# Performance work log

Hardware: AMD Instinct MI355X
Metric: run time of the kernel (lower is better)

The kernel has to match this reference:

```python
import jax, jax.numpy as jnp
import numpy as np

PATCH_SIZE = 16
PATCH_STRIDE = 8
LEVEL = 3

# pywt db4 decomposition filters (dec_lo, dec_hi)
_DB4_DEC_LO = np.array([-0.010597401784997278, 0.032883011666982945,
                        0.030841381835986965, -0.18703481171888114,
                        -0.02798376941698385, 0.6308807679295904,
                        0.7148465705525415, 0.23037781330885523], dtype=np.float32)
_DB4_DEC_HI = np.array([-0.23037781330885523, 0.7148465705525415,
                        -0.6308807679295904, -0.02798376941698385,
                        0.18703481171888114, 0.030841381835986965,
                        -0.032883011666982945, -0.010597401784997278], dtype=np.float32)


def _swt(x, level):
    """Undecimated (a-trous) SWT with periodic boundary, ptwt convention.
    x: (BN, T) with T divisible by 2**level. Returns [cA_L, cD_L, ..., cD_1]."""
    # torch conv1d is cross-correlation -> use flipped filters (true convolution)
    filt = jnp.stack([jnp.asarray(_DB4_DEC_LO[::-1].copy()),
                      jnp.asarray(_DB4_DEC_HI[::-1].copy())], axis=0)[:, None, :]  # (2,1,8)
    filt = filt.astype(x.dtype)
    flen = filt.shape[-1]
    res_lo = x[:, None, :]  # (BN, 1, T)
    details = []
    for lvl in range(level):
        d = 2 ** lvl
        padl, padr = d * (flen // 2 - 1), d * (flen // 2)
        xp = jnp.concatenate([res_lo[..., -padl:], res_lo, res_lo[..., :padr]], axis=-1)
        res = jax.lax.conv_general_dilated(
            xp, filt, window_strides=(1,), padding='VALID',
            rhs_dilation=(d,), dimension_numbers=('NCH', 'OIH', 'NCH'))  # (BN,2,T)
        res_lo = res[:, :1, :]
        details.append(res[:, 1, :])
    return [res_lo[:, 0, :]] + details[::-1]


def setup_inputs() -> dict:
    key = jax.random.key(0)
    x = jax.random.normal(key, (64, 4096, 32), dtype=jnp.float32)
    return {"x": x}


def reference(x):
    B, T, N = x.shape
    xt = jnp.transpose(x, (0, 2, 1))  # (B, N, T)
    pow2 = 2 ** LEVEL
    pad_len = (-T) % pow2
    if pad_len:
        xt = jnp.pad(xt, ((0, 0), (0, 0), (0, pad_len)), mode='edge')  # replicate
    T_pad = T + pad_len
    coeffs = _swt(xt.reshape(B * N, T_pad), LEVEL)           # (level+1) x (BN, T_pad)
    cs = jnp.stack(coeffs, axis=1).reshape(B, N, LEVEL + 1, T_pad)
    if pad_len:
        cs = cs[..., :T]
    P = (T - PATCH_SIZE) // PATCH_STRIDE + 1
    idx = jnp.arange(P)[:, None] * PATCH_STRIDE + jnp.arange(PATCH_SIZE)[None, :]
    patches = cs[..., idx]                                   # (B, N, L+1, P, p)
    patches = jnp.transpose(patches, (0, 3, 1, 2, 4))        # (B, P, N, L+1, p)
    return patches.reshape(B * P, N * (LEVEL + 1), PATCH_SIZE)
```

## Files before the change

### kernel.cpp

```cpp
#include <hip/hip_runtime.h>


#define NTHREADS 256
#define T_MASK   4095

#define S_IN  132
#define S_A1  116
#define S_A2  108
#define S_ST  76
#define OFF_IN 0
#define OFF_A1 4224
#define OFF_A2 0
#define OFF_ST 7936
#define ST_C   2436
#define LDS_FLOATS (OFF_ST + 4*ST_C)

__device__ __constant__ float c_lo[8] = {
    -0.010597401784997278f, 0.032883011666982945f, 0.030841381835986965f,
    -0.18703481171888114f, -0.02798376941698385f, 0.6308807679295904f,
    0.7148465705525415f,   0.23037781330885523f};
__device__ __constant__ float c_hi[8] = {
    -0.23037781330885523f, 0.7148465705525415f, -0.6308807679295904f,
    -0.02798376941698385f, 0.18703481171888114f, 0.030841381835986965f,
    -0.032883011666982945f, -0.010597401784997278f};

__global__ __launch_bounds__(NTHREADS, 2) void swt_patch(const float* __restrict__ x,
                                                         float* __restrict__ out) {
    __shared__ float lds[LDS_FLOATS];

    const int blk = blockIdx.x;
    const int b   = blk >> 6;
    const int cid = blk & 63;
    const int T0  = cid << 6;
    const int p0  = cid << 3;
    const int tid = threadIdx.x;

    const float* xb = x + (size_t)b * (4096 * 32);
    {
#pragma unroll
        for (int it = 0; it < 4; ++it) {
            const int id = tid + it * NTHREADS;
            const int i  = id >> 3;
            const int n0 = (id & 7) * 4;
            const int t  = (T0 - 23 + i) & T_MASK;
            const float4 v = *(const float4*)&xb[(size_t)t * 32 + n0];
            lds[OFF_IN + (n0 + 0) * S_IN + i] = v.x;
            lds[OFF_IN + (n0 + 1) * S_IN + i] = v.y;
            lds[OFF_IN + (n0 + 2) * S_IN + i] = v.z;
            lds[OFF_IN + (n0 + 3) * S_IN + i] = v.w;
        }
    }
    __syncthreads();

    for (int tsk = tid; tsk < 29 * 32; tsk += NTHREADS) {
        const int n = tsk & 31, q = tsk >> 5;
        const int trel0 = -20 + 4 * q;
        float w[12];
        const int base = OFF_IN + n * S_IN + 4 * q;
        *(float4*)&w[0] = *(const float4*)&lds[base];
        *(float4*)&w[4] = *(const float4*)&lds[base + 4];
        *(float4*)&w[8] = *(const float4*)&lds[base + 8];
        float4 va, vd;
        float* pa = (float*)&va; float* pd = (float*)&vd;
#pragma unroll
        for (int ii = 0; ii < 4; ++ii) {
            float sa = 0.f, sd = 0.f;
#pragma unroll
            for (int j = 0; j < 8; ++j) {
                const float v = w[ii + 7 - j];
                sa = fmaf(c_lo[j], v, sa);
                sd = fmaf(c_hi[j], v, sd);
            }
            pa[ii] = sa; pd[ii] = sd;
        }
        *(float4*)&lds[OFF_A1 + n * S_A1 + (trel0 + 20)] = va;
        if (trel0 >= 0 && trel0 <= 68)
            *(float4*)&lds[OFF_ST + 3 * ST_C + n * S_ST + trel0] = vd;
    }
    __syncthreads();

    for (int tsk = tid; tsk < 25 * 32; tsk += NTHREADS) {
        const int n = tsk & 31, q = tsk >> 5;
        const int trel0 = -12 + 4 * q;
        float w[20];
        const int base = OFF_A1 + n * S_A1 + 4 * q;
#pragma unroll
        for (int c4 = 0; c4 < 5; ++c4)
            *(float4*)&w[4 * c4] = *(const float4*)&lds[base + 4 * c4];
        float4 va, vd;
        float* pa = (float*)&va; float* pd = (float*)&vd;
#pragma unroll
        for (int ii = 0; ii < 4; ++ii) {
            float sa = 0.f, sd = 0.f;
#pragma unroll
            for (int j = 0; j < 8; ++j) {
                const float v = w[ii + 16 - 2 * j];
                sa = fmaf(c_lo[j], v, sa);
                sd = fmaf(c_hi[j], v, sd);
            }
            pa[ii] = sa; pd[ii] = sd;
        }
        *(float4*)&lds[OFF_A2 + n * S_A2 + (trel0 + 12)] = va;
        if (trel0 >= 0 && trel0 <= 68)
            *(float4*)&lds[OFF_ST + 2 * ST_C + n * S_ST + trel0] = vd;
    }
    __syncthreads();

    for (int tsk = tid; tsk < 18 * 32; tsk += NTHREADS) {
        const int n = tsk & 31, q = tsk >> 5;
        const int trel0 = 4 * q;
        float w[32];
        const int base = OFF_A2 + n * S_A2 + trel0;
#pragma unroll
        for (int c4 = 0; c4 < 8; ++c4)
            *(float4*)&w[4 * c4] = *(const float4*)&lds[base + 4 * c4];
        float4 va, vd;
        float* pa = (float*)&va; float* pd = (float*)&vd;
#pragma unroll
        for (int ii = 0; ii < 4; ++ii) {
            float sa = 0.f, sd = 0.f;
#pragma unroll
            for (int j = 0; j < 8; ++j) {
                const float v = w[ii + 28 - 4 * j];
                sa = fmaf(c_lo[j], v, sa);
                sd = fmaf(c_hi[j], v, sd);
            }
            pa[ii] = sa; pd[ii] = sd;
        }
        *(float4*)&lds[OFF_ST + 0 * ST_C + n * S_ST + trel0] = va;
        *(float4*)&lds[OFF_ST + 1 * ST_C + n * S_ST + trel0] = vd;
    }
    __syncthreads();

    float4* out4 = (float4*)(out + ((size_t)b * 511 + p0) * 2048);
#pragma unroll
    for (int it = 0; it < 16; ++it) {
        const int e4 = tid + it * NTHREADS;
        const int p_local = e4 >> 9;
        if (p0 + p_local < 511) {
            const int n  = (e4 >> 4) & 31;
            const int c  = (e4 >> 2) & 3;
            const int trel = 8 * p_local + 4 * (e4 & 3);
            out4[e4] = *(const float4*)&lds[OFF_ST + c * ST_C + n * S_ST + trel];
        }
    }
}

extern "C" void kernel_launch(void* const* d_in, const int* in_sizes, int n_in,
                              void* d_out, int out_size, void* d_ws, size_t ws_size,
                              hipStream_t stream) {
    const float* x = (const float*)d_in[0];
    float* out = (float*)d_out;
    hipLaunchKernelGGL(swt_patch, dim3(64 * 64), dim3(NTHREADS), 0, stream, x, out);
}
```

Before: 290.4 us.

## Write SWT coefficients directly to global patches, dropping LDS staging stage

Each level's detail coefficients (and the final approximation) are now written straight from registers to their one or two overlapping output patch slots in global memory. This removes the LDS staging buffer, its extra barrier and the final copy loop. The smaller LDS footprint and trimmed halo lets launch bounds rise to four blocks per SM for more occupancy. The cost is scattered float4 stores that are less contiguous than the previous coalesced patch-ordered write, plus some redundancy reduction in the halo compute.

```diff
diff --git a/kernel.cpp b/kernel.cpp
--- a/kernel.cpp
+++ b/kernel.cpp
@@ -4,16 +4,13 @@
 #define NTHREADS 256
 #define T_MASK   4095
 
-#define S_IN  132
-#define S_A1  116
-#define S_A2  108
-#define S_ST  76
+#define S_IN  116
+#define S_A1  108
+#define S_A2  92
 #define OFF_IN 0
-#define OFF_A1 4224
+#define OFF_A1 3712
 #define OFF_A2 0
-#define OFF_ST 7936
-#define ST_C   2436
-#define LDS_FLOATS (OFF_ST + 4*ST_C)
+#define LDS_FLOATS (OFF_A1 + 32 * S_A1)
 
 __device__ __constant__ float c_lo[8] = {
     -0.010597401784997278f, 0.032883011666982945f, 0.030841381835986965f,
@@ -24,7 +21,18 @@
     -0.02798376941698385f, 0.18703481171888114f, 0.030841381835986965f,
     -0.032883011666982945f, -0.010597401784997278f};
 
-__global__ __launch_bounds__(NTHREADS, 2) void swt_patch(const float* __restrict__ x,
+__device__ __forceinline__ void store_quad(float4* __restrict__ out4b, int t0,
+                                           int n, int c, const float4 v) {
+    const int p_hi  = t0 >> 3;
+    const int jq_hi = (t0 & 7) >> 2;
+    const int base  = n * 16 + c * 4 + jq_hi;
+    if (p_hi < 511)
+        out4b[(size_t)p_hi * 512 + base] = v;
+    if (p_hi > 0)
+        out4b[(size_t)(p_hi - 1) * 512 + base + 2] = v;
+}
+
+__global__ __launch_bounds__(NTHREADS, 4) void swt_patch(const float* __restrict__ x,
                                                          float* __restrict__ out) {
     __shared__ float lds[LDS_FLOATS];
 
@@ -32,27 +40,24 @@
     const int b   = blk >> 6;
     const int cid = blk & 63;
     const int T0  = cid << 6;
-    const int p0  = cid << 3;
     const int tid = threadIdx.x;
 
     const float* xb = x + (size_t)b * (4096 * 32);
-    {
-#pragma unroll
-        for (int it = 0; it < 4; ++it) {
-            const int id = tid + it * NTHREADS;
-            const int i  = id >> 3;
-            const int n0 = (id & 7) * 4;
-            const int t  = (T0 - 23 + i) & T_MASK;
-            const float4 v = *(const float4*)&xb[(size_t)t * 32 + n0];
-            lds[OFF_IN + (n0 + 0) * S_IN + i] = v.x;
-            lds[OFF_IN + (n0 + 1) * S_IN + i] = v.y;
-            lds[OFF_IN + (n0 + 2) * S_IN + i] = v.z;
-            lds[OFF_IN + (n0 + 3) * S_IN + i] = v.w;
-        }
+    float4* out4b = (float4*)out + (size_t)b * 511 * 512;
+
+    for (int id = tid; id < 928; id += NTHREADS) {
+        const int i  = id >> 3;
+        const int n0 = (id & 7) * 4;
+        const int t  = (T0 - 23 + i) & T_MASK;
+        const float4 v = *(const float4*)&xb[(size_t)t * 32 + n0];
+        lds[OFF_IN + (n0 + 0) * S_IN + i] = v.x;
+        lds[OFF_IN + (n0 + 1) * S_IN + i] = v.y;
+        lds[OFF_IN + (n0 + 2) * S_IN + i] = v.z;
+        lds[OFF_IN + (n0 + 3) * S_IN + i] = v.w;
     }
     __syncthreads();
 
-    for (int tsk = tid; tsk < 29 * 32; tsk += NTHREADS) {
+    for (int tsk = tid; tsk < 27 * 32; tsk += NTHREADS) {
         const int n = tsk & 31, q = tsk >> 5;
         const int trel0 = -20 + 4 * q;
         float w[12];
@@ -74,12 +79,12 @@
             pa[ii] = sa; pd[ii] = sd;
         }
         *(float4*)&lds[OFF_A1 + n * S_A1 + (trel0 + 20)] = va;
-        if (trel0 >= 0 && trel0 <= 68)
-            *(float4*)&lds[OFF_ST + 3 * ST_C + n * S_ST + trel0] = vd;
+        if (trel0 >= 0 && trel0 <= 60)
+            store_quad(out4b, T0 + trel0, n, 3, vd);
     }
     __syncthreads();
 
-    for (int tsk = tid; tsk < 25 * 32; tsk += NTHREADS) {
+    for (int tsk = tid; tsk < 23 * 32; tsk += NTHREADS) {
         const int n = tsk & 31, q = tsk >> 5;
         const int trel0 = -12 + 4 * q;
         float w[20];
@@ -101,12 +106,12 @@
             pa[ii] = sa; pd[ii] = sd;
         }
         *(float4*)&lds[OFF_A2 + n * S_A2 + (trel0 + 12)] = va;
-        if (trel0 >= 0 && trel0 <= 68)
-            *(float4*)&lds[OFF_ST + 2 * ST_C + n * S_ST + trel0] = vd;
+        if (trel0 >= 0 && trel0 <= 60)
+            store_quad(out4b, T0 + trel0, n, 2, vd);
     }
     __syncthreads();
 
-    for (int tsk = tid; tsk < 18 * 32; tsk += NTHREADS) {
+    for (int tsk = tid; tsk < 16 * 32; tsk += NTHREADS) {
         const int n = tsk & 31, q = tsk >> 5;
         const int trel0 = 4 * q;
         float w[32];
@@ -127,22 +132,8 @@
             }
             pa[ii] = sa; pd[ii] = sd;
         }
-        *(float4*)&lds[OFF_ST + 0 * ST_C + n * S_ST + trel0] = va;
-        *(float4*)&lds[OFF_ST + 1 * ST_C + n * S_ST + trel0] = vd;
-    }
-    __syncthreads();
-
-    float4* out4 = (float4*)(out + ((size_t)b * 511 + p0) * 2048);
-#pragma unroll
-    for (int it = 0; it < 16; ++it) {
-        const int e4 = tid + it * NTHREADS;
-        const int p_local = e4 >> 9;
-        if (p0 + p_local < 511) {
-            const int n  = (e4 >> 4) & 31;
-            const int c  = (e4 >> 2) & 3;
-            const int trel = 8 * p_local + 4 * (e4 & 3);
-            out4[e4] = *(const float4*)&lds[OFF_ST + c * ST_C + n * S_ST + trel];
-        }
+        store_quad(out4b, T0 + trel0, n, 0, va);
+        store_quad(out4b, T0 + trel0, n, 1, vd);
     }
 }
 
```

Result: slower. 391.7 us (+34.9%).

## Compute all three SWT levels in registers per thread, dropping intermediate LDS stages

Applied to the files above, without the earlier changes.

Each thread now owns one channel and a 9-sample output segment. It loads a 58-sample halo window straight from global memory into registers and computes the level-1, level-2 and level-3 approximations and details entirely in registers. Only the final coefficients go to LDS for the patch write-out. This removes the LDS staging of the input and intermediates and three barriers. In exchange it adds redundant halo computation, scalar strided global loads, and heavy register use (about 150 floats) that may spill or reduce occupancy.

```diff
diff --git a/kernel.cpp b/kernel.cpp
--- a/kernel.cpp
+++ b/kernel.cpp
@@ -4,16 +4,9 @@
 #define NTHREADS 256
 #define T_MASK   4095
 
-#define S_IN  132
-#define S_A1  116
-#define S_A2  108
-#define S_ST  76
-#define OFF_IN 0
-#define OFF_A1 4224
-#define OFF_A2 0
-#define OFF_ST 7936
-#define ST_C   2436
-#define LDS_FLOATS (OFF_ST + 4*ST_C)
+#define S_ST 76
+#define ST_C 2436
+#define LDS_FLOATS (4 * ST_C)
 
 __device__ __constant__ float c_lo[8] = {
     -0.010597401784997278f, 0.032883011666982945f, 0.030841381835986965f,
@@ -34,101 +27,80 @@
     const int T0  = cid << 6;
     const int p0  = cid << 3;
     const int tid = threadIdx.x;
+    const int n   = tid & 31;
+    const int s   = tid >> 5;
+    const int t0  = 9 * s;
 
-    const float* xb = x + (size_t)b * (4096 * 32);
-    {
+    const float* xb = x + (size_t)b * (4096 * 32) + n;
+
+    float xw[58];
+    if (cid != 0 && cid != 63) {
+        const float* xp = xb + (size_t)(T0 + t0 - 21) * 32;
 #pragma unroll
-        for (int it = 0; it < 4; ++it) {
-            const int id = tid + it * NTHREADS;
-            const int i  = id >> 3;
-            const int n0 = (id & 7) * 4;
-            const int t  = (T0 - 23 + i) & T_MASK;
-            const float4 v = *(const float4*)&xb[(size_t)t * 32 + n0];
-            lds[OFF_IN + (n0 + 0) * S_IN + i] = v.x;
-            lds[OFF_IN + (n0 + 1) * S_IN + i] = v.y;
-            lds[OFF_IN + (n0 + 2) * S_IN + i] = v.z;
-            lds[OFF_IN + (n0 + 3) * S_IN + i] = v.w;
+        for (int i = 0; i < 58; ++i) xw[i] = xp[(size_t)i * 32];
+    } else {
+#pragma unroll
+        for (int i = 0; i < 58; ++i) {
+            const int t = (T0 + t0 - 21 + i) & T_MASK;
+            xw[i] = xb[(size_t)t * 32];
         }
     }
-    __syncthreads();
 
-    for (int tsk = tid; tsk < 29 * 32; tsk += NTHREADS) {
-        const int n = tsk & 31, q = tsk >> 5;
-        const int trel0 = -20 + 4 * q;
-        float w[12];
-        const int base = OFF_IN + n * S_IN + 4 * q;
-        *(float4*)&w[0] = *(const float4*)&lds[base];
-        *(float4*)&w[4] = *(const float4*)&lds[base + 4];
-        *(float4*)&w[8] = *(const float4*)&lds[base + 8];
-        float4 va, vd;
-        float* pa = (float*)&va; float* pd = (float*)&vd;
+    {
+        float d1[9];
 #pragma unroll
-        for (int ii = 0; ii < 4; ++ii) {
-            float sa = 0.f, sd = 0.f;
+        for (int m = 0; m < 9; ++m) {
+            float sd = 0.f;
 #pragma unroll
-            for (int j = 0; j < 8; ++j) {
-                const float v = w[ii + 7 - j];
-                sa = fmaf(c_lo[j], v, sa);
-                sd = fmaf(c_hi[j], v, sd);
-            }
-            pa[ii] = sa; pd[ii] = sd;
+            for (int j = 0; j < 8; ++j) sd = fmaf(c_hi[j], xw[m + 25 - j], sd);
+            d1[m] = sd;
         }
-        *(float4*)&lds[OFF_A1 + n * S_A1 + (trel0 + 20)] = va;
-        if (trel0 >= 0 && trel0 <= 68)
-            *(float4*)&lds[OFF_ST + 3 * ST_C + n * S_ST + trel0] = vd;
+#pragma unroll
+        for (int m = 0; m < 9; ++m) lds[3 * ST_C + n * S_ST + t0 + m] = d1[m];
     }
-    __syncthreads();
 
-    for (int tsk = tid; tsk < 25 * 32; tsk += NTHREADS) {
-        const int n = tsk & 31, q = tsk >> 5;
-        const int trel0 = -12 + 4 * q;
-        float w[20];
-        const int base = OFF_A1 + n * S_A1 + 4 * q;
+    float a1[51];
 #pragma unroll
-        for (int c4 = 0; c4 < 5; ++c4)
-            *(float4*)&w[4 * c4] = *(const float4*)&lds[base + 4 * c4];
-        float4 va, vd;
-        float* pa = (float*)&va; float* pd = (float*)&vd;
+    for (int k = 0; k < 51; ++k) {
+        float sa = 0.f;
 #pragma unroll
-        for (int ii = 0; ii < 4; ++ii) {
-            float sa = 0.f, sd = 0.f;
+        for (int j = 0; j < 8; ++j) sa = fmaf(c_lo[j], xw[k + 7 - j], sa);
+        a1[k] = sa;
+    }
+
+    {
+        float d2[9];
 #pragma unroll
-            for (int j = 0; j < 8; ++j) {
-                const float v = w[ii + 16 - 2 * j];
-                sa = fmaf(c_lo[j], v, sa);
-                sd = fmaf(c_hi[j], v, sd);
-            }
-            pa[ii] = sa; pd[ii] = sd;
+        for (int m = 0; m < 9; ++m) {
+            float sd = 0.f;
+#pragma unroll
+            for (int j = 0; j < 8; ++j) sd = fmaf(c_hi[j], a1[m + 26 - 2 * j], sd);
+            d2[m] = sd;
         }
-        *(float4*)&lds[OFF_A2 + n * S_A2 + (trel0 + 12)] = va;
-        if (trel0 >= 0 && trel0 <= 68)
-            *(float4*)&lds[OFF_ST + 2 * ST_C + n * S_ST + trel0] = vd;
+#pragma unroll
+        for (int m = 0; m < 9; ++m) lds[2 * ST_C + n * S_ST + t0 + m] = d2[m];
     }
-    __syncthreads();
 
-    for (int tsk = tid; tsk < 18 * 32; tsk += NTHREADS) {
-        const int n = tsk & 31, q = tsk >> 5;
-        const int trel0 = 4 * q;
-        float w[32];
-        const int base = OFF_A2 + n * S_A2 + trel0;
+    float a2[37];
 #pragma unroll
-        for (int c4 = 0; c4 < 8; ++c4)
-            *(float4*)&w[4 * c4] = *(const float4*)&lds[base + 4 * c4];
-        float4 va, vd;
-        float* pa = (float*)&va; float* pd = (float*)&vd;
+    for (int m2 = 0; m2 < 37; ++m2) {
+        float sa = 0.f;
 #pragma unroll
-        for (int ii = 0; ii < 4; ++ii) {
-            float sa = 0.f, sd = 0.f;
+        for (int j = 0; j < 8; ++j) sa = fmaf(c_lo[j], a1[m2 + 14 - 2 * j], sa);
+        a2[m2] = sa;
+    }
+
 #pragma unroll
-            for (int j = 0; j < 8; ++j) {
-                const float v = w[ii + 28 - 4 * j];
-                sa = fmaf(c_lo[j], v, sa);
-                sd = fmaf(c_hi[j], v, sd);
-            }
-            pa[ii] = sa; pd[ii] = sd;
+    for (int m = 0; m < 9; ++m) {
+        float sa = 0.f, sd = 0.f;
+#pragma unroll
+        for (int j = 0; j < 8; ++j) {
+            const float v = a2[m + 28 - 4 * j];
+            sa = fmaf(c_lo[j], v, sa);
+            sd = fmaf(c_hi[j], v, sd);
         }
-        *(float4*)&lds[OFF_ST + 0 * ST_C + n * S_ST + trel0] = va;
-        *(float4*)&lds[OFF_ST + 1 * ST_C + n * S_ST + trel0] = vd;
+        lds[0 * ST_C + n * S_ST + t0 + m] = sa;
+        lds[1 * ST_C + n * S_ST + t0 + m] = sd;
     }
     __syncthreads();
 
@@ -138,10 +110,10 @@
         const int e4 = tid + it * NTHREADS;
         const int p_local = e4 >> 9;
         if (p0 + p_local < 511) {
-            const int n  = (e4 >> 4) & 31;
+            const int nn = (e4 >> 4) & 31;
             const int c  = (e4 >> 2) & 3;
             const int trel = 8 * p_local + 4 * (e4 & 3);
-            out4[e4] = *(const float4*)&lds[OFF_ST + c * ST_C + n * S_ST + trel];
+            out4[e4] = *(const float4*)&lds[c * ST_C + nn * S_ST + trel];
         }
     }
 }
```

Measured after the change: 289.0 us. About the same (-0.5%).
